# Performance work log

Hardware: AMD Instinct MI355X
Metric: run time of the kernel (lower is better)

The kernel has to match this reference:

```python
import jax, jax.numpy as jnp
import numpy as np

B, N, C, H = 2, 2048, 1024, 16
D = C // H  # head_dim = 64


def setup_inputs() -> dict:
    key = jax.random.key(0)
    k1, k2, k3, k4 = jax.random.split(key, 4)
    x = jax.random.normal(k1, (B, N, C), dtype=jnp.float32)
    # params (torch Linear: y = x @ W.T + b). Store as [in, out] for einsum.
    w_qkv = jax.random.normal(k2, (C, 3 * C), dtype=jnp.float32) * (1.0 / np.sqrt(C))
    w_out = jax.random.normal(k3, (C, C), dtype=jnp.float32) * (1.0 / np.sqrt(C))
    b_out = jax.random.normal(k4, (C,), dtype=jnp.float32) * 0.01
    # causal mask: 1 above the diagonal -> masked_fill(-inf)
    attn_mask = jnp.triu(jnp.ones((N, N), dtype=jnp.int32), k=1)
    return {"x": x, "w_qkv": w_qkv, "w_out": w_out, "b_out": b_out, "attn_mask": attn_mask}


def reference(x, w_qkv, w_out, b_out, attn_mask):
    b, n, c = x.shape
    scale = 1.0 / jnp.sqrt(jnp.asarray(D, dtype=x.dtype))
    qkv = jnp.einsum('bnc,cd->bnd', x, w_qkv)                # [B, N, 3C]
    qkv = qkv.reshape(b, n, 3, H, D)
    q = qkv[:, :, 0].transpose(0, 2, 1, 3)                   # [B, H, N, D]
    k = qkv[:, :, 1].transpose(0, 2, 1, 3)
    v = qkv[:, :, 2].transpose(0, 2, 1, 3)
    scores = jnp.einsum('bhqd,bhkd->bhqk', q, k) * scale     # [B, H, N, N]
    scores = jnp.where(attn_mask == 1, jnp.asarray(-jnp.inf, dtype=scores.dtype), scores)
    attn = jax.nn.softmax(scores, axis=-1)
    # dropout is identity in eval mode (deterministic reference)
    out = jnp.einsum('bhqk,bhkd->bhqd', attn, v)             # [B, H, N, D]
    out = out.transpose(0, 2, 1, 3).reshape(b, n, c)         # [B, N, C]
    return jnp.einsum('bnc,cd->bnd', out, w_out) + b_out
```

## Files before the change

kernel.cpp:

```cpp
#include <hip/hip_runtime.h>

typedef _Float16 f16;
typedef _Float16 f16x8 __attribute__((ext_vector_type(8)));
typedef _Float16 f16x4 __attribute__((ext_vector_type(4)));
typedef float    f32x4 __attribute__((ext_vector_type(4)));

#define MFMA16(a, b, c) __builtin_amdgcn_mfma_f32_16x16x32_f16((a), (b), (c), 0, 0, 0)

__device__ __forceinline__ void gload16(const void* g, void* l) {
  __builtin_amdgcn_global_load_lds(
      (const __attribute__((address_space(1))) unsigned int*)g,
      (__attribute__((address_space(3))) unsigned int*)l, 16, 0, 0);
}

__device__ __forceinline__ float ex2(float x) {
  float r;
  asm("v_exp_f32 %0, %1" : "=v"(r) : "v"(x));
  return r;
}

#define WAITV(N) asm volatile("s_waitcnt vmcnt(" #N ")" ::: "memory")
#define BARRIER() __builtin_amdgcn_s_barrier()
#define CFENCE() asm volatile("" ::: "memory")


__global__ void cast_f32_f16(const float* __restrict__ in, f16* __restrict__ out, int n4) {
  int i = blockIdx.x * blockDim.x + threadIdx.x;
  if (i < n4) {
    float4 v = ((const float4*)in)[i];
    f16x4 o;
    o.x = (f16)v.x; o.y = (f16)v.y; o.z = (f16)v.z; o.w = (f16)v.w;
    ((f16x4*)out)[i] = o;
  }
}

__global__ void transpose_cast(const float* __restrict__ in, f16* __restrict__ out, int R, int Cc) {
  __shared__ float tile[32][33];
  int c0 = blockIdx.x * 32, r0 = blockIdx.y * 32;
  int tx = threadIdx.x, ty = threadIdx.y;
#pragma unroll
  for (int i = ty; i < 32; i += 8)
    tile[i][tx] = in[(size_t)(r0 + i) * Cc + c0 + tx];
  __syncthreads();
#pragma unroll
  for (int i = ty; i < 32; i += 8)
    out[(size_t)(c0 + i) * R + r0 + tx] = (f16)tile[tx][i];
}

template <int KDIM>
__device__ __forceinline__ void gemm_core(const f16* __restrict__ A, const f16* __restrict__ Bt,
                                          int bm, int bn, f16* lA, f16* lB, f32x4 acc[4][4]) {
  const int t = threadIdx.x, lane = t & 63, wave = t >> 6;
  const int wm = wave >> 1, wn = wave & 1;
  const int srow = lane >> 3;
  const int skb = (lane & 7) * 16;
  const int nkt = KDIM / 64;
  for (int kt = 0; kt < nkt; ++kt) {
    __syncthreads();
#pragma unroll
    for (int c = 0; c < 4; ++c) {
      int cc = c * 4 + wave;
      int row = cc * 8 + srow;
      int kbs = skb ^ ((row & 7) << 4);
      gload16((const char*)A + (size_t)(bm * 128 + row) * (KDIM * 2) + kt * 128 + kbs,
              lA + cc * 512);
      gload16((const char*)Bt + (size_t)(bn * 128 + row) * (KDIM * 2) + kt * 128 + kbs,
              lB + cc * 512);
    }
    __syncthreads();
#pragma unroll
    for (int ks = 0; ks < 2; ++ks) {
      f16x8 af[4], bf[4];
#pragma unroll
      for (int mi = 0; mi < 4; ++mi) {
        int r = wm * 64 + mi * 16 + (lane & 15);
        int ke = (ks * 32 + ((lane >> 4) << 3)) ^ ((r & 7) << 3);
        af[mi] = *(const f16x8*)&lA[r * 64 + ke];
      }
#pragma unroll
      for (int ni = 0; ni < 4; ++ni) {
        int r = wn * 64 + ni * 16 + (lane & 15);
        int ke = (ks * 32 + ((lane >> 4) << 3)) ^ ((r & 7) << 3);
        bf[ni] = *(const f16x8*)&lB[r * 64 + ke];
      }
#pragma unroll
      for (int mi = 0; mi < 4; ++mi)
#pragma unroll
        for (int ni = 0; ni < 4; ++ni)
          acc[mi][ni] = MFMA16(af[mi], bf[ni], acc[mi][ni]);
    }
  }
}

__global__ __launch_bounds__(256, 2) void gemm_qkv(const f16* __restrict__ A,
                                                   const f16* __restrict__ Bt,
                                                   f16* __restrict__ Qo, f16* __restrict__ Ko,
                                                   f16* __restrict__ Vt) {
  __shared__ __align__(16) f16 smem[128 * 136];
  f16* lA = smem;
  f16* lB = smem + 8192;
  f32x4 acc[4][4] = {};
  int w = blockIdx.x;
  int xcd = w & 7, i = w >> 3;
  int xr = xcd >> 1, xc = xcd & 1;
  int bm = xr * 8 + (i & 7);
  int bn = xc * 12 + (i >> 3);
  gemm_core<1024>(A, Bt, bm, bn, lA, lB, acc);
  int lane = threadIdx.x & 63, wave = threadIdx.x >> 6;
  int wm = wave >> 1, wn = wave & 1;
  int g = lane >> 4, q15 = lane & 15;
  int sec = (bn * 128) >> 10;
  if (sec < 2) {
    float scl = (sec == 0) ? 0.18033688f : 1.0f;
#pragma unroll
    for (int mi = 0; mi < 4; ++mi)
#pragma unroll
      for (int ni = 0; ni < 4; ++ni)
#pragma unroll
        for (int reg = 0; reg < 4; ++reg) {
          int gr = bm * 128 + wm * 64 + mi * 16 + (g << 2) + reg;
          int gc = bn * 128 + wn * 64 + ni * 16 + q15;
          int b = gr >> 11, n = gr & 2047;
          int jj = gc & 1023;
          int h = jj >> 6, d = jj & 63;
          f16 v = (f16)(acc[mi][ni][reg] * scl);
          size_t bh = (size_t)(b * 16 + h);
          if (sec == 0) Qo[(bh * 2048 + n) * 64 + d] = v;
          else          Ko[(bh * 2048 + n) * 64 + d] = v;
        }
  } else {
    __syncthreads();
#pragma unroll
    for (int mi = 0; mi < 4; ++mi)
#pragma unroll
      for (int ni = 0; ni < 4; ++ni)
#pragma unroll
        for (int reg = 0; reg < 4; ++reg) {
          int rl = wm * 64 + mi * 16 + (g << 2) + reg;
          int cl = wn * 64 + ni * 16 + q15;
          int r5 = rl & 31;
          int rlp = (rl & ~31) | (((r5 >> 2) & 3) << 3) | (((r5 >> 4) & 1) << 2) | (r5 & 3);
          smem[cl * 136 + rlp] = (f16)acc[mi][ni][reg];
        }
    __syncthreads();
    int tid = threadIdx.x;
    int cl = tid >> 1, half = tid & 1;
    int jj = (bn * 128 + cl) & 1023;
    int h = jj >> 6, d = jj & 63;
    int b = (bm * 128) >> 11;
    size_t bh = (size_t)(b * 16 + h);
    f16* dst = Vt + (bh * 64 + d) * 2048 + (bm * 128 & 2047) + half * 64;
    const f16* src = smem + cl * 136 + half * 64;
#pragma unroll
    for (int j8 = 0; j8 < 8; ++j8)
      *(f16x8*)&dst[j8 * 8] = *(const f16x8*)&src[j8 * 8];
  }
}

__device__ __forceinline__ void attn_one(const f16* __restrict__ Qb, const f16* __restrict__ Kb,
                                         const f16* __restrict__ Vb, f16* __restrict__ Ob,
                                         int qt, int lane, int wave, f16* lK, f16* lV) {
  const int N = 2048;
  const int wq0 = qt * 64 + wave * 16;
  const int g = lane >> 4, q15 = lane & 15;
  f16x8 qf[2];
#pragma unroll
  for (int ks = 0; ks < 2; ++ks)
    qf[ks] = *(const f16x8*)&Qb[(size_t)(wq0 + q15) * 64 + ks * 32 + (g << 3)];
  f32x4 oacc[4] = {};
  float mrun = -1e30f, lrun = 0.f;
  const int srow = lane >> 3, skb = (lane & 7) * 16;
  const int ntiles = qt + 1;

  auto STAGE = [&](int buf, int kv) {
    int kv0 = kv << 6;
#pragma unroll
    for (int c = 0; c < 2; ++c) {
      int cc = c * 4 + wave;
      int row = cc * 8 + srow;
      int kbs = skb ^ ((row & 7) << 4);
      gload16((const char*)Kb + (size_t)(kv0 + row) * 128 + kbs, lK + buf * 4096 + cc * 512);
      gload16((const char*)Vb + (size_t)row * (N * 2) + (size_t)kv0 * 2 + kbs,
              lV + buf * 4096 + cc * 512);
    }
  };

  STAGE(0, 0);
  if (ntiles > 1) STAGE(1, 1);
  for (int kv = 0; kv < ntiles; ++kv) {
    int cur = kv & 1;
    if (kv + 1 < ntiles) WAITV(4); else WAITV(0);
    BARRIER();
    const f16* K0 = lK + cur * 4096;
    const f16* V0 = lV + cur * 4096;
    int kv0 = kv << 6;
    f32x4 s[4] = {};
    __builtin_amdgcn_s_setprio(1);
#pragma unroll
    for (int ks = 0; ks < 2; ++ks) {
      f16x8 kf[4];
#pragma unroll
      for (int ni = 0; ni < 4; ++ni) {
        int r = ni * 16 + q15;
        int ke = (ks * 32 + (g << 3)) ^ ((r & 7) << 3);
        kf[ni] = *(const f16x8*)&K0[r * 64 + ke];
      }
#pragma unroll
      for (int ni = 0; ni < 4; ++ni) s[ni] = MFMA16(kf[ni], qf[ks], s[ni]);
    }
    __builtin_amdgcn_s_setprio(0);
    if (kv == qt) {
      int gq = wq0 + q15;
#pragma unroll
      for (int ni = 0; ni < 4; ++ni)
#pragma unroll
        for (int reg = 0; reg < 4; ++reg) {
          int gk = kv0 + ni * 16 + g * 4 + reg;
          if (gk > gq) s[ni][reg] = -1e30f;
        }
    }
    f32x4 m4 = s[0];
#pragma unroll
    for (int ni = 1; ni < 4; ++ni)
#pragma unroll
      for (int reg = 0; reg < 4; ++reg) m4[reg] = fmaxf(m4[reg], s[ni][reg]);
    float mx = fmaxf(fmaxf(m4[0], m4[1]), fmaxf(m4[2], m4[3]));
    mx = fmaxf(mx, __shfl_xor(mx, 16));
    mx = fmaxf(mx, __shfl_xor(mx, 32));
    if (__any(mx > mrun)) {
      float mnew = fmaxf(mrun, mx);
      float corr = ex2(mrun - mnew);
      mrun = mnew;
      lrun *= corr;
#pragma unroll
      for (int ni = 0; ni < 4; ++ni)
#pragma unroll
        for (int reg = 0; reg < 4; ++reg) oacc[ni][reg] *= corr;
    }
#pragma unroll
    for (int ni = 0; ni < 4; ++ni)
#pragma unroll
      for (int reg = 0; reg < 4; ++reg) s[ni][reg] = ex2(s[ni][reg] - mrun);
    f32x4 racc = (s[0] + s[1]) + (s[2] + s[3]);
    float rsum = (racc[0] + racc[1]) + (racc[2] + racc[3]);
    rsum += __shfl_xor(rsum, 16);
    rsum += __shfl_xor(rsum, 32);
    lrun += rsum;
    f16x8 pf[2];
#pragma unroll
    for (int ks = 0; ks < 2; ++ks)
#pragma unroll
      for (int e = 0; e < 8; ++e) pf[ks][e] = (f16)s[2 * ks + (e >> 2)][e & 3];
    __builtin_amdgcn_s_setprio(1);
#pragma unroll
    for (int ks = 0; ks < 2; ++ks) {
      f16x8 vf[4];
#pragma unroll
      for (int mi = 0; mi < 4; ++mi) {
        int r = mi * 16 + q15;
        int ke = (ks * 32 + (g << 3)) ^ ((r & 7) << 3);
        vf[mi] = *(const f16x8*)&V0[r * 64 + ke];
      }
#pragma unroll
      for (int mi = 0; mi < 4; ++mi) oacc[mi] = MFMA16(vf[mi], pf[ks], oacc[mi]);
    }
    __builtin_amdgcn_s_setprio(0);
    BARRIER();
    CFENCE();
    if (kv + 2 < ntiles) STAGE(cur, kv + 2);
  }
  float inv = 1.0f / lrun;
  int gq = wq0 + q15;
#pragma unroll
  for (int mi = 0; mi < 4; ++mi) {
    f16x4 o4;
#pragma unroll
    for (int reg = 0; reg < 4; ++reg) o4[reg] = (f16)(oacc[mi][reg] * inv);
    *(f16x4*)&Ob[(size_t)gq * 1024 + mi * 16 + g * 4] = o4;
  }
}

__global__ __launch_bounds__(256, 4) void attn(const f16* __restrict__ Q,
                                               const f16* __restrict__ K,
                                               const f16* __restrict__ Vt,
                                               f16* __restrict__ O) {
  __shared__ __align__(16) f16 lK[2 * 4096];
  __shared__ __align__(16) f16 lV[2 * 4096];
  int w = blockIdx.x;
  int c = w & 7, j = w >> 3;
  int bh = c * 4 + (j & 3);
  int qt = 31 - (j >> 2);
  int b = bh >> 4, h = bh & 15;
  int lane = threadIdx.x & 63, wave = threadIdx.x >> 6;
  const f16* Qb = Q + (size_t)bh * 2048 * 64;
  const f16* Kb = K + (size_t)bh * 2048 * 64;
  const f16* Vb = Vt + (size_t)bh * 2048 * 64;
  f16* Ob = O + (size_t)b * 2048 * 1024 + h * 64;
  attn_one(Qb, Kb, Vb, Ob, qt, lane, wave, lK, lV);
}

__global__ __launch_bounds__(256, 2) void gemm_out(const f16* __restrict__ A,
                                                   const f16* __restrict__ Bt,
                                                   const float* __restrict__ bias,
                                                   float* __restrict__ out) {
  __shared__ __align__(16) f16 lA[128 * 64];
  __shared__ __align__(16) f16 lB[128 * 64];
  f32x4 acc[4][4] = {};
  int w = blockIdx.x;
  int xcd = w & 7, i = w >> 3;
  int bm = xcd * 4 + (i & 3);
  int bn = i >> 2;
  gemm_core<1024>(A, Bt, bm, bn, lA, lB, acc);
  int lane = threadIdx.x & 63, wave = threadIdx.x >> 6;
  int wm = wave >> 1, wn = wave & 1;
#pragma unroll
  for (int mi = 0; mi < 4; ++mi)
#pragma unroll
    for (int ni = 0; ni < 4; ++ni)
#pragma unroll
      for (int reg = 0; reg < 4; ++reg) {
        int gr = bm * 128 + wm * 64 + mi * 16 + ((lane >> 4) << 2) + reg;
        int gc = bn * 128 + wn * 64 + ni * 16 + (lane & 15);
        out[(size_t)gr * 1024 + gc] = acc[mi][ni][reg] + bias[gc];
      }
}

extern "C" void kernel_launch(void* const* d_in, const int* in_sizes, int n_in,
                              void* d_out, int out_size, void* d_ws, size_t ws_size,
                              hipStream_t stream) {
  const float* x     = (const float*)d_in[0];
  const float* w_qkv = (const float*)d_in[1];
  const float* w_out = (const float*)d_in[2];
  const float* b_out = (const float*)d_in[3];
  float* out = (float*)d_out;
  char* ws = (char*)d_ws;

  f16* xh    = (f16*)(ws);
  f16* wqkvT = (f16*)(ws + (8u << 20));
  f16* woutT = (f16*)(ws + (14u << 20));
  f16* Qs    = (f16*)(ws + (16u << 20));
  f16* Ks    = (f16*)(ws + (24u << 20));
  f16* Vts   = (f16*)(ws + (32u << 20));
  f16* Oa    = (f16*)(ws + (40u << 20));

  cast_f32_f16<<<4096, 256, 0, stream>>>(x, xh, 1048576);
  transpose_cast<<<dim3(96, 32), dim3(32, 8), 0, stream>>>(w_qkv, wqkvT, 1024, 3072);
  transpose_cast<<<dim3(32, 32), dim3(32, 8), 0, stream>>>(w_out, woutT, 1024, 1024);
  gemm_qkv<<<768, 256, 0, stream>>>(xh, wqkvT, Qs, Ks, Vts);
  attn<<<1024, 256, 0, stream>>>(Qs, Ks, Vts, Oa);
  gemm_out<<<256, 256, 0, stream>>>(Oa, woutT, b_out, out);
}
```

Baseline: 106.4 us.

## Pair complementary causal query tiles per block to balance work and share K/V loads

Each attention block now handles two query tiles, qa and 31-qa, from the same head. This gives every block the same amount of causal work and lets the two tiles share each staged K/V tile in LDS. The grid is halved to 512 blocks and launch bounds drop to 2 blocks per CU, since each thread now holds two sets of accumulators. The cost is higher register pressure and less parallelism, and the block-to-head mapping changes.

```diff
diff --git a/kernel.cpp b/kernel.cpp
--- a/kernel.cpp
+++ b/kernel.cpp
@@ -157,20 +157,22 @@
   }
 }
 
-__device__ __forceinline__ void attn_one(const f16* __restrict__ Qb, const f16* __restrict__ Kb,
-                                         const f16* __restrict__ Vb, f16* __restrict__ Ob,
-                                         int qt, int lane, int wave, f16* lK, f16* lV) {
+__device__ __forceinline__ void attn_pair(const f16* __restrict__ Qb, const f16* __restrict__ Kb,
+                                          const f16* __restrict__ Vb, f16* __restrict__ Ob,
+                                          int qa, int qb, int lane, int wave, f16* lK, f16* lV) {
   const int N = 2048;
-  const int wq0 = qt * 64 + wave * 16;
   const int g = lane >> 4, q15 = lane & 15;
-  f16x8 qf[2];
-#pragma unroll
-  for (int ks = 0; ks < 2; ++ks)
-    qf[ks] = *(const f16x8*)&Qb[(size_t)(wq0 + q15) * 64 + ks * 32 + (g << 3)];
-  f32x4 oacc[4] = {};
-  float mrun = -1e30f, lrun = 0.f;
+  const int wqA = qa * 64 + wave * 16, wqB = qb * 64 + wave * 16;
+  f16x8 qfA[2], qfB[2];
+#pragma unroll
+  for (int ks = 0; ks < 2; ++ks) {
+    qfA[ks] = *(const f16x8*)&Qb[(size_t)(wqA + q15) * 64 + ks * 32 + (g << 3)];
+    qfB[ks] = *(const f16x8*)&Qb[(size_t)(wqB + q15) * 64 + ks * 32 + (g << 3)];
+  }
+  f32x4 oA[4] = {}, oB[4] = {};
+  float mA = -1e30f, lAr = 0.f, mB = -1e30f, lBr = 0.f;
   const int srow = lane >> 3, skb = (lane & 7) * 16;
-  const int ntiles = qt + 1;
+  const int nt = qb + 1;
 
   auto STAGE = [&](int buf, int kv) {
     int kv0 = kv << 6;
@@ -186,15 +188,15 @@
   };
 
   STAGE(0, 0);
-  if (ntiles > 1) STAGE(1, 1);
-  for (int kv = 0; kv < ntiles; ++kv) {
+  STAGE(1, 1);
+  for (int kv = 0; kv < nt; ++kv) {
     int cur = kv & 1;
-    if (kv + 1 < ntiles) WAITV(4); else WAITV(0);
+    if (kv + 1 < nt) WAITV(4); else WAITV(0);
     BARRIER();
     const f16* K0 = lK + cur * 4096;
     const f16* V0 = lV + cur * 4096;
-    int kv0 = kv << 6;
-    f32x4 s[4] = {};
+    const bool actA = (kv <= qa);
+    f32x4 sA[4] = {}, sB[4] = {};
     __builtin_amdgcn_s_setprio(1);
 #pragma unroll
     for (int ks = 0; ks < 2; ++ks) {
@@ -206,51 +208,98 @@
         kf[ni] = *(const f16x8*)&K0[r * 64 + ke];
       }
 #pragma unroll
-      for (int ni = 0; ni < 4; ++ni) s[ni] = MFMA16(kf[ni], qf[ks], s[ni]);
+      for (int ni = 0; ni < 4; ++ni) sB[ni] = MFMA16(kf[ni], qfB[ks], sB[ni]);
+      if (actA) {
+#pragma unroll
+        for (int ni = 0; ni < 4; ++ni) sA[ni] = MFMA16(kf[ni], qfA[ks], sA[ni]);
+      }
     }
     __builtin_amdgcn_s_setprio(0);
-    if (kv == qt) {
-      int gq = wq0 + q15;
-#pragma unroll
-      for (int ni = 0; ni < 4; ++ni)
-#pragma unroll
-        for (int reg = 0; reg < 4; ++reg) {
-          int gk = kv0 + ni * 16 + g * 4 + reg;
-          if (gk > gq) s[ni][reg] = -1e30f;
-        }
-    }
-    f32x4 m4 = s[0];
-#pragma unroll
-    for (int ni = 1; ni < 4; ++ni)
-#pragma unroll
-      for (int reg = 0; reg < 4; ++reg) m4[reg] = fmaxf(m4[reg], s[ni][reg]);
-    float mx = fmaxf(fmaxf(m4[0], m4[1]), fmaxf(m4[2], m4[3]));
-    mx = fmaxf(mx, __shfl_xor(mx, 16));
-    mx = fmaxf(mx, __shfl_xor(mx, 32));
-    if (__any(mx > mrun)) {
-      float mnew = fmaxf(mrun, mx);
-      float corr = ex2(mrun - mnew);
-      mrun = mnew;
-      lrun *= corr;
-#pragma unroll
-      for (int ni = 0; ni < 4; ++ni)
-#pragma unroll
-        for (int reg = 0; reg < 4; ++reg) oacc[ni][reg] *= corr;
-    }
-#pragma unroll
-    for (int ni = 0; ni < 4; ++ni)
-#pragma unroll
-      for (int reg = 0; reg < 4; ++reg) s[ni][reg] = ex2(s[ni][reg] - mrun);
-    f32x4 racc = (s[0] + s[1]) + (s[2] + s[3]);
-    float rsum = (racc[0] + racc[1]) + (racc[2] + racc[3]);
-    rsum += __shfl_xor(rsum, 16);
-    rsum += __shfl_xor(rsum, 32);
-    lrun += rsum;
-    f16x8 pf[2];
-#pragma unroll
-    for (int ks = 0; ks < 2; ++ks)
-#pragma unroll
-      for (int e = 0; e < 8; ++e) pf[ks][e] = (f16)s[2 * ks + (e >> 2)][e & 3];
+    int kv0 = kv << 6;
+    if (kv == qb) {
+      int gq = wqB + q15;
+#pragma unroll
+      for (int ni = 0; ni < 4; ++ni)
+#pragma unroll
+        for (int reg = 0; reg < 4; ++reg)
+          if (kv0 + ni * 16 + g * 4 + reg > gq) sB[ni][reg] = -1e30f;
+    }
+    if (actA && kv == qa) {
+      int gq = wqA + q15;
+#pragma unroll
+      for (int ni = 0; ni < 4; ++ni)
+#pragma unroll
+        for (int reg = 0; reg < 4; ++reg)
+          if (kv0 + ni * 16 + g * 4 + reg > gq) sA[ni][reg] = -1e30f;
+    }
+    f16x8 pfB[2];
+    {
+      f32x4 m4 = sB[0];
+#pragma unroll
+      for (int ni = 1; ni < 4; ++ni)
+#pragma unroll
+        for (int reg = 0; reg < 4; ++reg) m4[reg] = fmaxf(m4[reg], sB[ni][reg]);
+      float mx = fmaxf(fmaxf(m4[0], m4[1]), fmaxf(m4[2], m4[3]));
+      mx = fmaxf(mx, __shfl_xor(mx, 16));
+      mx = fmaxf(mx, __shfl_xor(mx, 32));
+      if (__any(mx > mB)) {
+        float mnew = fmaxf(mB, mx);
+        float corr = ex2(mB - mnew);
+        mB = mnew;
+        lBr *= corr;
+#pragma unroll
+        for (int ni = 0; ni < 4; ++ni)
+#pragma unroll
+          for (int reg = 0; reg < 4; ++reg) oB[ni][reg] *= corr;
+      }
+#pragma unroll
+      for (int ni = 0; ni < 4; ++ni)
+#pragma unroll
+        for (int reg = 0; reg < 4; ++reg) sB[ni][reg] = ex2(sB[ni][reg] - mB);
+      f32x4 racc = (sB[0] + sB[1]) + (sB[2] + sB[3]);
+      float rsum = (racc[0] + racc[1]) + (racc[2] + racc[3]);
+      rsum += __shfl_xor(rsum, 16);
+      rsum += __shfl_xor(rsum, 32);
+      lBr += rsum;
+#pragma unroll
+      for (int ks = 0; ks < 2; ++ks)
+#pragma unroll
+        for (int e = 0; e < 8; ++e) pfB[ks][e] = (f16)sB[2 * ks + (e >> 2)][e & 3];
+    }
+    f16x8 pfA[2];
+    if (actA) {
+      f32x4 m4 = sA[0];
+#pragma unroll
+      for (int ni = 1; ni < 4; ++ni)
+#pragma unroll
+        for (int reg = 0; reg < 4; ++reg) m4[reg] = fmaxf(m4[reg], sA[ni][reg]);
+      float mx = fmaxf(fmaxf(m4[0], m4[1]), fmaxf(m4[2], m4[3]));
+      mx = fmaxf(mx, __shfl_xor(mx, 16));
+      mx = fmaxf(mx, __shfl_xor(mx, 32));
+      if (__any(mx > mA)) {
+        float mnew = fmaxf(mA, mx);
+        float corr = ex2(mA - mnew);
+        mA = mnew;
+        lAr *= corr;
+#pragma unroll
+        for (int ni = 0; ni < 4; ++ni)
+#pragma unroll
+          for (int reg = 0; reg < 4; ++reg) oA[ni][reg] *= corr;
+      }
+#pragma unroll
+      for (int ni = 0; ni < 4; ++ni)
+#pragma unroll
+        for (int reg = 0; reg < 4; ++reg) sA[ni][reg] = ex2(sA[ni][reg] - mA);
+      f32x4 racc = (sA[0] + sA[1]) + (sA[2] + sA[3]);
+      float rsum = (racc[0] + racc[1]) + (racc[2] + racc[3]);
+      rsum += __shfl_xor(rsum, 16);
+      rsum += __shfl_xor(rsum, 32);
+      lAr += rsum;
+#pragma unroll
+      for (int ks = 0; ks < 2; ++ks)
+#pragma unroll
+        for (int e = 0; e < 8; ++e) pfA[ks][e] = (f16)sA[2 * ks + (e >> 2)][e & 3];
+    }
     __builtin_amdgcn_s_setprio(1);
 #pragma unroll
     for (int ks = 0; ks < 2; ++ks) {
@@ -262,25 +311,42 @@
         vf[mi] = *(const f16x8*)&V0[r * 64 + ke];
       }
 #pragma unroll
-      for (int mi = 0; mi < 4; ++mi) oacc[mi] = MFMA16(vf[mi], pf[ks], oacc[mi]);
+      for (int mi = 0; mi < 4; ++mi) oB[mi] = MFMA16(vf[mi], pfB[ks], oB[mi]);
+      if (actA) {
+#pragma unroll
+        for (int mi = 0; mi < 4; ++mi) oA[mi] = MFMA16(vf[mi], pfA[ks], oA[mi]);
+      }
     }
     __builtin_amdgcn_s_setprio(0);
     BARRIER();
     CFENCE();
-    if (kv + 2 < ntiles) STAGE(cur, kv + 2);
-  }
-  float inv = 1.0f / lrun;
-  int gq = wq0 + q15;
-#pragma unroll
-  for (int mi = 0; mi < 4; ++mi) {
-    f16x4 o4;
-#pragma unroll
-    for (int reg = 0; reg < 4; ++reg) o4[reg] = (f16)(oacc[mi][reg] * inv);
-    *(f16x4*)&Ob[(size_t)gq * 1024 + mi * 16 + g * 4] = o4;
-  }
-}
-
-__global__ __launch_bounds__(256, 4) void attn(const f16* __restrict__ Q,
+    if (kv + 2 < nt) STAGE(cur, kv + 2);
+  }
+  {
+    float inv = 1.0f / lBr;
+    int gq = wqB + q15;
+#pragma unroll
+    for (int mi = 0; mi < 4; ++mi) {
+      f16x4 o4;
+#pragma unroll
+      for (int reg = 0; reg < 4; ++reg) o4[reg] = (f16)(oB[mi][reg] * inv);
+      *(f16x4*)&Ob[(size_t)gq * 1024 + mi * 16 + g * 4] = o4;
+    }
+  }
+  {
+    float inv = 1.0f / lAr;
+    int gq = wqA + q15;
+#pragma unroll
+    for (int mi = 0; mi < 4; ++mi) {
+      f16x4 o4;
+#pragma unroll
+      for (int reg = 0; reg < 4; ++reg) o4[reg] = (f16)(oA[mi][reg] * inv);
+      *(f16x4*)&Ob[(size_t)gq * 1024 + mi * 16 + g * 4] = o4;
+    }
+  }
+}
+
+__global__ __launch_bounds__(256, 2) void attn(const f16* __restrict__ Q,
                                                const f16* __restrict__ K,
                                                const f16* __restrict__ Vt,
                                                f16* __restrict__ O) {
@@ -288,15 +354,17 @@
   __shared__ __align__(16) f16 lV[2 * 4096];
   int w = blockIdx.x;
   int c = w & 7, j = w >> 3;
-  int bh = c * 4 + (j & 3);
-  int qt = 31 - (j >> 2);
+  int bh = c * 4 + (j >> 4);
+  int jm = j & 15;
+  int x = (j < 32) ? jm : 15 - jm;
+  int qa = x, qb = 31 - x;
   int b = bh >> 4, h = bh & 15;
   int lane = threadIdx.x & 63, wave = threadIdx.x >> 6;
   const f16* Qb = Q + (size_t)bh * 2048 * 64;
   const f16* Kb = K + (size_t)bh * 2048 * 64;
   const f16* Vb = Vt + (size_t)bh * 2048 * 64;
   f16* Ob = O + (size_t)b * 2048 * 1024 + h * 64;
-  attn_one(Qb, Kb, Vb, Ob, qt, lane, wave, lK, lV);
+  attn_pair(Qb, Kb, Vb, Ob, qa, qb, lane, wave, lK, lV);
 }
 
 __global__ __launch_bounds__(256, 2) void gemm_out(const f16* __restrict__ A,
@@ -347,6 +415,6 @@
   transpose_cast<<<dim3(96, 32), dim3(32, 8), 0, stream>>>(w_qkv, wqkvT, 1024, 3072);
   transpose_cast<<<dim3(32, 32), dim3(32, 8), 0, stream>>>(w_out, woutT, 1024, 1024);
   gemm_qkv<<<768, 256, 0, stream>>>(xh, wqkvT, Qs, Ks, Vts);
-  attn<<<1024, 256, 0, stream>>>(Qs, Ks, Vts, Oa);
+  attn<<<512, 256, 0, stream>>>(Qs, Ks, Vts, Oa);
   gemm_out<<<256, 256, 0, stream>>>(Oa, woutT, b_out, out);
 }
```

New measurement: 113.8 us. 6.9% more time.

## Fuse x fp32-to-fp16 cast into QKV GEMM loads and rebalance attention schedule

Applied to the files above, without the earlier changes.

Removes the separate cast kernel for x: the QKV GEMM now streams fp32 x tiles straight into LDS with a swizzled layout and converts them to fp16 in registers before the MFMAs. This drops one kernel launch and the fp16 write and re-read of x, but doubles the LDS footprint and global traffic for the A tile, and the new loop is single-buffered with a barrier each k-step. The attention grid mapping is also changed so causal query tiles are interleaved in ascending and descending order across heads, to balance work across CUs.

```diff
diff --git a/kernel.cpp b/kernel.cpp
--- a/kernel.cpp
+++ b/kernel.cpp
@@ -23,16 +23,6 @@
 #define BARRIER() __builtin_amdgcn_s_barrier()
 #define CFENCE() asm volatile("" ::: "memory")
 
-
-__global__ void cast_f32_f16(const float* __restrict__ in, f16* __restrict__ out, int n4) {
-  int i = blockIdx.x * blockDim.x + threadIdx.x;
-  if (i < n4) {
-    float4 v = ((const float4*)in)[i];
-    f16x4 o;
-    o.x = (f16)v.x; o.y = (f16)v.y; o.z = (f16)v.z; o.w = (f16)v.w;
-    ((f16x4*)out)[i] = o;
-  }
-}
 
 __global__ void transpose_cast(const float* __restrict__ in, f16* __restrict__ out, int R, int Cc) {
   __shared__ float tile[32][33];
@@ -92,23 +82,76 @@
   }
 }
 
-__global__ __launch_bounds__(256, 2) void gemm_qkv(const f16* __restrict__ A,
+__global__ __launch_bounds__(256, 2) void gemm_qkv(const float* __restrict__ X,
                                                    const f16* __restrict__ Bt,
                                                    f16* __restrict__ Qo, f16* __restrict__ Ko,
                                                    f16* __restrict__ Vt) {
-  __shared__ __align__(16) f16 smem[128 * 136];
-  f16* lA = smem;
-  f16* lB = smem + 8192;
+  __shared__ __align__(16) char smem[49152];
+  float* lA = (float*)smem;
+  f16* lB = (f16*)(smem + 32768);
+  f16* tb = (f16*)smem;
   f32x4 acc[4][4] = {};
   int w = blockIdx.x;
   int xcd = w & 7, i = w >> 3;
   int xr = xcd >> 1, xc = xcd & 1;
   int bm = xr * 8 + (i & 7);
   int bn = xc * 12 + (i >> 3);
-  gemm_core<1024>(A, Bt, bm, bn, lA, lB, acc);
-  int lane = threadIdx.x & 63, wave = threadIdx.x >> 6;
-  int wm = wave >> 1, wn = wave & 1;
-  int g = lane >> 4, q15 = lane & 15;
+  const int t = threadIdx.x, lane = t & 63, wave = t >> 6;
+  const int wm = wave >> 1, wn = wave & 1;
+  const int g = lane >> 4, q15 = lane & 15;
+  {
+    const int srowB = lane >> 3, skbB = (lane & 7) * 16;
+    const int srowA = lane >> 4, sltA = lane & 15;
+    for (int kt = 0; kt < 16; ++kt) {
+      __syncthreads();
+#pragma unroll
+      for (int c = 0; c < 8; ++c) {
+        int cc = c * 4 + wave;
+        int row = cc * 4 + srowA;
+        int sw = ((row & 3) << 5) | (((row >> 2) & 1) << 4);
+        int kbs = (sltA * 16) ^ sw;
+        gload16((const char*)X + (size_t)(bm * 128 + row) * 4096 + kt * 256 + kbs,
+                (char*)lA + cc * 1024);
+      }
+#pragma unroll
+      for (int c = 0; c < 4; ++c) {
+        int cc = c * 4 + wave;
+        int row = cc * 8 + srowB;
+        int kbs = skbB ^ ((row & 7) << 4);
+        gload16((const char*)Bt + (size_t)(bn * 128 + row) * 2048 + kt * 128 + kbs,
+                lB + cc * 512);
+      }
+      __syncthreads();
+#pragma unroll
+      for (int ks = 0; ks < 2; ++ks) {
+        f16x8 af[4], bf[4];
+#pragma unroll
+        for (int mi = 0; mi < 4; ++mi) {
+          int r = wm * 64 + mi * 16 + q15;
+          int sw = ((r & 3) << 5) | (((r >> 2) & 1) << 4);
+          int b0 = r * 256 + ((ks * 128 + g * 32) ^ sw);
+          f32x4 a0 = *(const f32x4*)((const char*)lA + b0);
+          f32x4 a1 = *(const f32x4*)((const char*)lA + (b0 ^ 16));
+#pragma unroll
+          for (int e = 0; e < 4; ++e) {
+            af[mi][e] = (f16)a0[e];
+            af[mi][4 + e] = (f16)a1[e];
+          }
+        }
+#pragma unroll
+        for (int ni = 0; ni < 4; ++ni) {
+          int r = wn * 64 + ni * 16 + q15;
+          int ke = (ks * 32 + (g << 3)) ^ ((r & 7) << 3);
+          bf[ni] = *(const f16x8*)&lB[r * 64 + ke];
+        }
+#pragma unroll
+        for (int mi = 0; mi < 4; ++mi)
+#pragma unroll
+          for (int ni = 0; ni < 4; ++ni)
+            acc[mi][ni] = MFMA16(af[mi], bf[ni], acc[mi][ni]);
+      }
+    }
+  }
   int sec = (bn * 128) >> 10;
   if (sec < 2) {
     float scl = (sec == 0) ? 0.18033688f : 1.0f;
@@ -140,7 +183,7 @@
           int cl = wn * 64 + ni * 16 + q15;
           int r5 = rl & 31;
           int rlp = (rl & ~31) | (((r5 >> 2) & 3) << 3) | (((r5 >> 4) & 1) << 2) | (r5 & 3);
-          smem[cl * 136 + rlp] = (f16)acc[mi][ni][reg];
+          tb[cl * 136 + rlp] = (f16)acc[mi][ni][reg];
         }
     __syncthreads();
     int tid = threadIdx.x;
@@ -150,7 +193,7 @@
     int b = (bm * 128) >> 11;
     size_t bh = (size_t)(b * 16 + h);
     f16* dst = Vt + (bh * 64 + d) * 2048 + (bm * 128 & 2047) + half * 64;
-    const f16* src = smem + cl * 136 + half * 64;
+    const f16* src = tb + cl * 136 + half * 64;
 #pragma unroll
     for (int j8 = 0; j8 < 8; ++j8)
       *(f16x8*)&dst[j8 * 8] = *(const f16x8*)&src[j8 * 8];
@@ -288,8 +331,10 @@
   __shared__ __align__(16) f16 lV[2 * 4096];
   int w = blockIdx.x;
   int c = w & 7, j = w >> 3;
-  int bh = c * 4 + (j & 3);
-  int qt = 31 - (j >> 2);
+  int a = j >> 5, k = j & 31;
+  int bh = c * 4 + a;
+  int kk = (a >= 2) ? ((k + 8) & 31) : k;
+  int qt = (a & 1) ? (31 - kk) : kk;
   int b = bh >> 4, h = bh & 15;
   int lane = threadIdx.x & 63, wave = threadIdx.x >> 6;
   const f16* Qb = Q + (size_t)bh * 2048 * 64;
@@ -335,7 +380,6 @@
   float* out = (float*)d_out;
   char* ws = (char*)d_ws;
 
-  f16* xh    = (f16*)(ws);
   f16* wqkvT = (f16*)(ws + (8u << 20));
   f16* woutT = (f16*)(ws + (14u << 20));
   f16* Qs    = (f16*)(ws + (16u << 20));
@@ -343,10 +387,9 @@
   f16* Vts   = (f16*)(ws + (32u << 20));
   f16* Oa    = (f16*)(ws + (40u << 20));
 
-  cast_f32_f16<<<4096, 256, 0, stream>>>(x, xh, 1048576);
   transpose_cast<<<dim3(96, 32), dim3(32, 8), 0, stream>>>(w_qkv, wqkvT, 1024, 3072);
   transpose_cast<<<dim3(32, 32), dim3(32, 8), 0, stream>>>(w_out, woutT, 1024, 1024);
-  gemm_qkv<<<768, 256, 0, stream>>>(xh, wqkvT, Qs, Ks, Vts);
+  gemm_qkv<<<768, 256, 0, stream>>>(x, wqkvT, Qs, Ks, Vts);
   attn<<<1024, 256, 0, stream>>>(Qs, Ks, Vts, Oa);
   gemm_out<<<256, 256, 0, stream>>>(Oa, woutT, b_out, out);
 }
```

Result: slower. 113.4 us (+6.6%).
